# Kernel tuning notes

Measured on AMD Instinct MI355X. Metric: run time of the kernel, lower is better.

The kernel has to match this reference:

```python
import jax, jax.numpy as jnp
import numpy as np

BETA = 1.0          # params['beta'] -> max_thres
MEM_LEN = 131072    # params['memory_len']
IN_DIM = 256
OUT_DIM = 2 * IN_DIM


def setup_inputs() -> dict:
    key = jax.random.key(0)
    ks = jax.random.split(key, 7)
    x = jax.random.normal(ks[0], (1, IN_DIM), dtype=jnp.float32)
    W_enc = jax.random.normal(ks[1], (IN_DIM, OUT_DIM), dtype=jnp.float32) * 0.05
    b_enc = jnp.zeros((OUT_DIM,), dtype=jnp.float32)
    memory = jax.random.normal(ks[2], (MEM_LEN, OUT_DIM), dtype=jnp.float32)
    mem_data = jax.random.normal(ks[3], (MEM_LEN, IN_DIM), dtype=jnp.float32)
    mean = jax.random.normal(ks[4], (IN_DIM,), dtype=jnp.float32) * 0.1
    std = jax.random.uniform(ks[5], (IN_DIM,), dtype=jnp.float32, minval=0.5, maxval=1.5)
    count = 5  # python int: current write cursor into the ring-buffer memory
    return {"x": x, "W_enc": W_enc, "b_enc": b_enc, "memory": memory,
            "mem_data": mem_data, "mean": mean, "std": std, "count": count}


def reference(x, W_enc, b_enc, memory, mem_data, mean, std, count):
    # normalize; zero out features with std == 0 (as in call())
    new = jnp.where(std == 0, jnp.zeros_like(x), (x - mean) / std)  # (1, in_dim)
    # Dense encoder with log_softmax activation
    enc = jax.nn.log_softmax(new @ W_enc + b_enc, axis=-1)          # (1, out_dim)
    # L1 distance to every memory row, then min  (tf.norm(..., ord=1, axis=1).min())
    dists = jnp.sum(jnp.abs(memory - enc), axis=1)                  # (mem_len,)
    loss = jnp.min(dists)
    # update_memory: if loss <= beta, overwrite slot (count % mem_len)
    pos = count % MEM_LEN
    do_update = loss <= BETA
    memory_new = jnp.where(do_update, memory.at[pos].set(enc[0]), memory)
    mem_data_new = jnp.where(do_update, mem_data.at[pos].set(x[0]), mem_data)
    return loss, memory_new, mem_data_new
```

## Files before the change

kernel.cpp:

```cpp
#include <hip/hip_runtime.h>

#define MEM_LEN 131072
#define IN_DIM 256
#define OUT_DIM 512
#define BETA 1.0f


__global__ __launch_bounds__(512) void k_encode(
    const float* __restrict__ x, const float* __restrict__ W,
    const float* __restrict__ b, const float* __restrict__ mean,
    const float* __restrict__ stdv, float* __restrict__ ws)
{
    __shared__ float s_new[IN_DIM];
    __shared__ float s_wred[8];
    __shared__ float s_bcast;
    const int tid = threadIdx.x;
    const int lane = tid & 63;
    const int wave = tid >> 6;

    if (tid < IN_DIM) {
        float sd = stdv[tid];
        s_new[tid] = (sd == 0.0f) ? 0.0f : (x[tid] - mean[tid]) / sd;
    }
    __syncthreads();

    float z = b[tid];
    #pragma unroll 8
    for (int k = 0; k < IN_DIM; ++k)
        z = fmaf(s_new[k], W[k * OUT_DIM + tid], z);

    float m = z;
    #pragma unroll
    for (int off = 32; off > 0; off >>= 1)
        m = fmaxf(m, __shfl_down(m, off, 64));
    if (lane == 0) s_wred[wave] = m;
    __syncthreads();
    if (tid == 0) {
        float mm = s_wred[0];
        for (int w = 1; w < 8; ++w) mm = fmaxf(mm, s_wred[w]);
        s_bcast = mm;
    }
    __syncthreads();
    const float zmax = s_bcast;

    float e = expf(z - zmax);
    float ssum = e;
    #pragma unroll
    for (int off = 32; off > 0; off >>= 1)
        ssum += __shfl_down(ssum, off, 64);
    __syncthreads();
    if (lane == 0) s_wred[wave] = ssum;
    __syncthreads();
    if (tid == 0) {
        float tot = 0.0f;
        for (int w = 0; w < 8; ++w) tot += s_wred[w];
        s_bcast = logf(tot);
        ((unsigned int*)ws)[512] = 0x7F800000u;
    }
    __syncthreads();
    const float lse = s_bcast;

    ws[tid] = z - zmax - lse;
}

__global__ __launch_bounds__(256) void k_dist_copy(
    const float* __restrict__ memory, const float* __restrict__ mem_data,
    float* __restrict__ out, const float* __restrict__ ws)
{
    __shared__ alignas(16) float s_enc[OUT_DIM];
    __shared__ float s_min[4];
    const int tid = threadIdx.x;
    const int lane = tid & 63;
    const int wave = tid >> 6;

    s_enc[tid] = ws[tid];
    s_enc[256 + tid] = ws[256 + tid];
    __syncthreads();

    const float4 e0 = ((const float4*)s_enc)[lane];
    const float4 e1 = ((const float4*)s_enc)[64 + lane];

    const int gwave = blockIdx.x * 4 + wave;
    const int n_waves = gridDim.x * 4;

    float wmin = INFINITY;
    float* const out_mem = out + 1;

    for (int r = gwave; r < MEM_LEN; r += n_waves) {
        const float4* src = (const float4*)(memory + (size_t)r * OUT_DIM);
        const float4 a0 = src[lane];
        const float4 a1 = src[64 + lane];

        float s = fabsf(a0.x - e0.x) + fabsf(a0.y - e0.y)
                + fabsf(a0.z - e0.z) + fabsf(a0.w - e0.w)
                + fabsf(a1.x - e1.x) + fabsf(a1.y - e1.y)
                + fabsf(a1.z - e1.z) + fabsf(a1.w - e1.w);

        float* dst = out_mem + (size_t)r * OUT_DIM;
        const int o0 = lane * 4;
        dst[o0 + 0] = a0.x; dst[o0 + 1] = a0.y; dst[o0 + 2] = a0.z; dst[o0 + 3] = a0.w;
        dst[256 + o0 + 0] = a1.x; dst[256 + o0 + 1] = a1.y;
        dst[256 + o0 + 2] = a1.z; dst[256 + o0 + 3] = a1.w;

        #pragma unroll
        for (int off = 32; off > 0; off >>= 1)
            s += __shfl_down(s, off, 64);
        if (lane == 0) wmin = fminf(wmin, s);
    }

    if (lane == 0) s_min[wave] = wmin;
    __syncthreads();
    if (tid == 0) {
        float bm = fminf(fminf(s_min[0], s_min[1]), fminf(s_min[2], s_min[3]));
        atomicMin((unsigned int*)ws + 512, __float_as_uint(bm));
    }

    const size_t total4 = (size_t)MEM_LEN * IN_DIM / 4;
    const size_t stride = (size_t)gridDim.x * 256;
    float* const out_md = out + 1 + (size_t)MEM_LEN * OUT_DIM;
    const float4* src4 = (const float4*)mem_data;
    for (size_t i = (size_t)blockIdx.x * 256 + tid; i < total4; i += stride) {
        const float4 v = src4[i];
        out_md[i * 4 + 0] = v.x; out_md[i * 4 + 1] = v.y;
        out_md[i * 4 + 2] = v.z; out_md[i * 4 + 3] = v.w;
    }
}

__global__ __launch_bounds__(512) void k_finalize(
    const float* __restrict__ x, const int* __restrict__ count,
    float* __restrict__ out, const float* __restrict__ ws)
{
    const int tid = threadIdx.x;
    const float loss = __uint_as_float(((const unsigned int*)ws)[512]);
    if (tid == 0) out[0] = loss;
    if (loss <= BETA) {
        int pos = count[0] % MEM_LEN;
        if (pos < 0) pos += MEM_LEN;
        out[1 + (size_t)pos * OUT_DIM + tid] = ws[tid];
        if (tid < IN_DIM)
            out[1 + (size_t)MEM_LEN * OUT_DIM + (size_t)pos * IN_DIM + tid] = x[tid];
    }
}

extern "C" void kernel_launch(void* const* d_in, const int* in_sizes, int n_in,
                              void* d_out, int out_size, void* d_ws, size_t ws_size,
                              hipStream_t stream) {
    const float* x        = (const float*)d_in[0];
    const float* W_enc    = (const float*)d_in[1];
    const float* b_enc    = (const float*)d_in[2];
    const float* memory   = (const float*)d_in[3];
    const float* mem_data = (const float*)d_in[4];
    const float* mean     = (const float*)d_in[5];
    const float* stdv     = (const float*)d_in[6];
    const int*   count    = (const int*)d_in[7];
    float* out = (float*)d_out;
    float* ws  = (float*)d_ws;

    k_encode<<<1, 512, 0, stream>>>(x, W_enc, b_enc, mean, stdv, ws);
    k_dist_copy<<<2048, 256, 0, stream>>>(memory, mem_data, out, ws);
    k_finalize<<<1, 512, 0, stream>>>(x, count, out, ws);
}
```

Baseline: 687.7 us.

## Split encoder GEMV across blocks and use nontemporal vector copies in dist kernel

The single-block encoder GEMV becomes a 16-block split-K partial-sum kernel followed by a small reduction and log-softmax kernel, so the encode step is no longer serial on one CU. The distance/copy kernel now gives each wave a contiguous run of 16 rows and 1024 float4 chunks. It uses nontemporal 16-byte loads and stores in place of scalar stores, aiming for better streaming bandwidth on the large memory copies. This adds an extra kernel launch, and the contiguous indexing hardcodes the 2048-block grid size.

```diff
diff --git a/kernel.cpp b/kernel.cpp
--- a/kernel.cpp
+++ b/kernel.cpp
@@ -4,30 +4,50 @@
 #define IN_DIM 256
 #define OUT_DIM 512
 #define BETA 1.0f
+#define NSLICE 16
+#define KSLICE (IN_DIM / NSLICE)
+
+typedef float v4  __attribute__((vector_size(16)));
+typedef float v4u __attribute__((vector_size(16), aligned(4)));
 
 
-__global__ __launch_bounds__(512) void k_encode(
+__global__ __launch_bounds__(512) void k_enc1(
     const float* __restrict__ x, const float* __restrict__ W,
-    const float* __restrict__ b, const float* __restrict__ mean,
-    const float* __restrict__ stdv, float* __restrict__ ws)
+    const float* __restrict__ mean, const float* __restrict__ stdv,
+    float* __restrict__ ws)
 {
-    __shared__ float s_new[IN_DIM];
+    __shared__ float s_new[KSLICE];
+    const int tid = threadIdx.x;
+    const int b = blockIdx.x;
+    const int k0 = b * KSLICE;
+
+    if (tid < KSLICE) {
+        const int k = k0 + tid;
+        const float sd = stdv[k];
+        s_new[tid] = (sd == 0.0f) ? 0.0f : (x[k] - mean[k]) / sd;
+    }
+    __syncthreads();
+
+    float acc = 0.0f;
+    #pragma unroll
+    for (int kk = 0; kk < KSLICE; ++kk)
+        acc = fmaf(s_new[kk], W[(size_t)(k0 + kk) * OUT_DIM + tid], acc);
+    ws[1024 + b * OUT_DIM + tid] = acc;
+}
+
+__global__ __launch_bounds__(512) void k_enc2(
+    const float* __restrict__ bias, float* __restrict__ ws)
+{
     __shared__ float s_wred[8];
     __shared__ float s_bcast;
     const int tid = threadIdx.x;
     const int lane = tid & 63;
     const int wave = tid >> 6;
 
-    if (tid < IN_DIM) {
-        float sd = stdv[tid];
-        s_new[tid] = (sd == 0.0f) ? 0.0f : (x[tid] - mean[tid]) / sd;
-    }
-    __syncthreads();
-
-    float z = b[tid];
-    #pragma unroll 8
-    for (int k = 0; k < IN_DIM; ++k)
-        z = fmaf(s_new[k], W[k * OUT_DIM + tid], z);
+    float z = bias[tid];
+    #pragma unroll
+    for (int s = 0; s < NSLICE; ++s)
+        z += ws[1024 + s * OUT_DIM + tid];
 
     float m = z;
     #pragma unroll
@@ -43,8 +63,7 @@
     __syncthreads();
     const float zmax = s_bcast;
 
-    float e = expf(z - zmax);
-    float ssum = e;
+    float ssum = expf(z - zmax);
     #pragma unroll
     for (int off = 32; off > 0; off >>= 1)
         ssum += __shfl_down(ssum, off, 64);
@@ -77,30 +96,29 @@
     s_enc[256 + tid] = ws[256 + tid];
     __syncthreads();
 
-    const float4 e0 = ((const float4*)s_enc)[lane];
-    const float4 e1 = ((const float4*)s_enc)[64 + lane];
+    const v4 e0 = ((const v4*)s_enc)[lane];
+    const v4 e1 = ((const v4*)s_enc)[64 + lane];
 
     const int gwave = blockIdx.x * 4 + wave;
-    const int n_waves = gridDim.x * 4;
-
     float wmin = INFINITY;
     float* const out_mem = out + 1;
 
-    for (int r = gwave; r < MEM_LEN; r += n_waves) {
-        const float4* src = (const float4*)(memory + (size_t)r * OUT_DIM);
-        const float4 a0 = src[lane];
-        const float4 a1 = src[64 + lane];
+    const int row0 = gwave * 16;
+    #pragma unroll 2
+    for (int rr = 0; rr < 16; ++rr) {
+        const int r = row0 + rr;
+        const v4* src = (const v4*)(memory + (size_t)r * OUT_DIM);
+        const v4 a0 = __builtin_nontemporal_load(src + lane);
+        const v4 a1 = __builtin_nontemporal_load(src + 64 + lane);
 
-        float s = fabsf(a0.x - e0.x) + fabsf(a0.y - e0.y)
-                + fabsf(a0.z - e0.z) + fabsf(a0.w - e0.w)
-                + fabsf(a1.x - e1.x) + fabsf(a1.y - e1.y)
-                + fabsf(a1.z - e1.z) + fabsf(a1.w - e1.w);
+        float s = fabsf(a0[0] - e0[0]) + fabsf(a0[1] - e0[1])
+                + fabsf(a0[2] - e0[2]) + fabsf(a0[3] - e0[3])
+                + fabsf(a1[0] - e1[0]) + fabsf(a1[1] - e1[1])
+                + fabsf(a1[2] - e1[2]) + fabsf(a1[3] - e1[3]);
 
         float* dst = out_mem + (size_t)r * OUT_DIM;
-        const int o0 = lane * 4;
-        dst[o0 + 0] = a0.x; dst[o0 + 1] = a0.y; dst[o0 + 2] = a0.z; dst[o0 + 3] = a0.w;
-        dst[256 + o0 + 0] = a1.x; dst[256 + o0 + 1] = a1.y;
-        dst[256 + o0 + 2] = a1.z; dst[256 + o0 + 3] = a1.w;
+        __builtin_nontemporal_store((v4u)a0, (v4u*)(dst + 4 * lane));
+        __builtin_nontemporal_store((v4u)a1, (v4u*)(dst + 256 + 4 * lane));
 
         #pragma unroll
         for (int off = 32; off > 0; off >>= 1)
@@ -115,14 +133,14 @@
         atomicMin((unsigned int*)ws + 512, __float_as_uint(bm));
     }
 
-    const size_t total4 = (size_t)MEM_LEN * IN_DIM / 4;
-    const size_t stride = (size_t)gridDim.x * 256;
     float* const out_md = out + 1 + (size_t)MEM_LEN * OUT_DIM;
-    const float4* src4 = (const float4*)mem_data;
-    for (size_t i = (size_t)blockIdx.x * 256 + tid; i < total4; i += stride) {
-        const float4 v = src4[i];
-        out_md[i * 4 + 0] = v.x; out_md[i * 4 + 1] = v.y;
-        out_md[i * 4 + 2] = v.z; out_md[i * 4 + 3] = v.w;
+    const v4* src4 = (const v4*)mem_data;
+    const size_t base4 = (size_t)gwave * 1024 + lane;
+    #pragma unroll 4
+    for (int it = 0; it < 16; ++it) {
+        const size_t i = base4 + (size_t)it * 64;
+        const v4 v = __builtin_nontemporal_load(src4 + i);
+        __builtin_nontemporal_store((v4u)v, (v4u*)(out_md + i * 4));
     }
 }
 
@@ -156,7 +174,8 @@
     float* out = (float*)d_out;
     float* ws  = (float*)d_ws;
 
-    k_encode<<<1, 512, 0, stream>>>(x, W_enc, b_enc, mean, stdv, ws);
+    k_enc1<<<NSLICE, 512, 0, stream>>>(x, W_enc, mean, stdv, ws);
+    k_enc2<<<1, 512, 0, stream>>>(b_enc, ws);
     k_dist_copy<<<2048, 256, 0, stream>>>(memory, mem_data, out, ws);
     k_finalize<<<1, 512, 0, stream>>>(x, count, out, ws);
 }
```

Measured after the change: 661.7 us. 1.04x faster.
